# Kernel tuning notes

Hardware: AMD Instinct MI355X
Metric: run time of the kernel (lower is better)

Reference implementation:

```python
import jax, jax.numpy as jnp
import numpy as np

N_NODES = 100000
N_EDGES = 1600000
D_IN = 256
D_OUT = 256


def _init_linear(key, out_f, in_f):
    # torch nn.Linear default: U(-1/sqrt(in_f), 1/sqrt(in_f))
    kw, kb = jax.random.split(key)
    bound = 1.0 / np.sqrt(in_f)
    W = jax.random.uniform(kw, (out_f, in_f), jnp.float32, -bound, bound)
    b = jax.random.uniform(kb, (out_f,), jnp.float32, -bound, bound)
    return W, b


def setup_inputs() -> dict:
    key = jax.random.key(0)
    ks = jax.random.split(key, 7)
    x = jax.random.normal(ks[0], (N_NODES, D_IN), jnp.float32)
    edge_index = jax.random.randint(ks[1], (2, N_EDGES), 0, N_NODES, jnp.int64)
    W1, b1 = _init_linear(ks[2], D_OUT, D_IN)
    W2, b2 = _init_linear(ks[3], D_OUT // 2, D_OUT)
    W3, b3 = _init_linear(ks[4], D_OUT // 2, D_OUT)
    Wd1, bd1 = _init_linear(ks[5], D_OUT, D_OUT)
    Wd2, bd2 = _init_linear(ks[6], 1, D_OUT)
    return {"x": x, "edge_index": edge_index,
            "W1": W1, "b1": b1, "W2": W2, "b2": b2, "W3": W3, "b3": b3,
            "Wd1": Wd1, "bd1": bd1, "Wd2": Wd2, "bd2": bd2}


def _l2norm(x):
    return x / jnp.linalg.norm(x, axis=-1, keepdims=True)


def reference(x, edge_index, W1, b1, W2, b2, W3, b3, Wd1, bd1, Wd2, bd2):
    src, dst = edge_index[0], edge_index[1]  # source_to_target flow
    x = jax.nn.relu(x @ W1.T + b1)           # [N, D_OUT]
    x = _l2norm(x)
    for _ in range(2):
        # sum-aggregate neighbor messages: scatter-add x[src] into dst
        nm = jax.ops.segment_sum(x[src], dst, num_segments=N_NODES)  # [N, D_OUT]
        x = jax.nn.relu(jnp.concatenate([x @ W2.T + b2, nm @ W3.T + b3], axis=-1))
        x = _l2norm(x)
    x = jax.nn.relu(x @ Wd1.T + bd1)
    return x @ Wd2.T + bd2                    # [N, 1]
```

## Files before the change

kernel.cpp:

```cpp
#include <hip/hip_runtime.h>
#include <math.h>


typedef _Float16 f16x8 __attribute__((ext_vector_type(8)));
typedef float    f32x16 __attribute__((ext_vector_type(16)));

constexpr int DIM = 256;
constexpr int BM  = 128;
constexpr int BK  = 32;
constexpr int SA  = 40;
constexpr int SW  = 40;

__device__ __forceinline__ unsigned pk_hi2(float a, float b) {
    unsigned short ha = __builtin_bit_cast(unsigned short, (_Float16)a);
    unsigned short hb = __builtin_bit_cast(unsigned short, (_Float16)b);
    return (unsigned)ha | ((unsigned)hb << 16);
}
__device__ __forceinline__ unsigned pk_lo2(float a, float b) {
    _Float16 ha = (_Float16)a, hb = (_Float16)b;
    unsigned short la = __builtin_bit_cast(unsigned short, (_Float16)(a - (float)ha));
    unsigned short lb = __builtin_bit_cast(unsigned short, (_Float16)(b - (float)hb));
    return (unsigned)la | ((unsigned)lb << 16);
}
__device__ __forceinline__ unsigned pack_pair(float v) {
    _Float16 hi = (_Float16)v;
    _Float16 lo = (_Float16)(v - (float)hi);
    return (unsigned)__builtin_bit_cast(unsigned short, hi)
         | ((unsigned)__builtin_bit_cast(unsigned short, lo) << 16);
}

template <int AMODE, int EPI>
__device__ __forceinline__
void gemm_body(const void* __restrict__ Av,
               const float* __restrict__ WA, const float* __restrict__ WB,
               const float* __restrict__ bA, const float* __restrict__ bB,
               void* __restrict__ outv,
               const float* __restrict__ wd2, const float* __restrict__ bd2,
               float* __restrict__ out1, int M)
{
    __shared__ __align__(16) _Float16 smem[30720];
    _Float16* As_hi = smem;
    _Float16* As_lo = smem + 5120;
    _Float16* Ws_hi = smem + 10240;
    _Float16* Ws_lo = smem + 20480;

    const int tid  = threadIdx.x;
    const int lane = tid & 63;
    const int w    = tid >> 6;
    const int rh   = w >> 1;
    const int ch   = w & 1;
    const int l31  = lane & 31;
    const int lh   = lane >> 5;
    const int bm0  = blockIdx.x * BM;

    const unsigned* Au = (const unsigned*)Av;
    const int srow = tid >> 3;
    const int sch  = (tid & 7) * 4;

    uint4  pa[4];
    float4 pw[8];

    auto fetchA = [&](int t) {
        const int k0 = t * BK;
        #pragma unroll
        for (int i = 0; i < 4; ++i) {
            const int gr = bm0 + srow + 32 * i;
            uint4 v = {0u, 0u, 0u, 0u};
            if (gr < M) v = *(const uint4*)&Au[(size_t)gr * 256 + k0 + sch];
            pa[i] = v;
        }
    };
    auto fetchW = [&](int t) {
        const int k0 = t * BK;
        #pragma unroll
        for (int i = 0; i < 8; ++i) {
            const int r = srow + 32 * i;
            const float* src = (r < 128) ? &WA[(size_t)r * 256]
                                         : &WB[(size_t)(r - 128) * 256];
            pw[i] = *(const float4*)&src[k0 + sch];
        }
    };
    auto stageA = [&]() {
        #pragma unroll
        for (int i = 0; i < 4; ++i) {
            const int r = srow + 32 * i;
            unsigned h0, h1, l0, l1;
            if (AMODE == 0) {
                const float x0 = __builtin_bit_cast(float, pa[i].x);
                const float x1 = __builtin_bit_cast(float, pa[i].y);
                const float x2 = __builtin_bit_cast(float, pa[i].z);
                const float x3 = __builtin_bit_cast(float, pa[i].w);
                h0 = pk_hi2(x0, x1); h1 = pk_hi2(x2, x3);
                l0 = pk_lo2(x0, x1); l1 = pk_lo2(x2, x3);
            } else {
                h0 = __builtin_amdgcn_perm(pa[i].y, pa[i].x, 0x05040100u);
                l0 = __builtin_amdgcn_perm(pa[i].y, pa[i].x, 0x07060302u);
                h1 = __builtin_amdgcn_perm(pa[i].w, pa[i].z, 0x05040100u);
                l1 = __builtin_amdgcn_perm(pa[i].w, pa[i].z, 0x07060302u);
            }
            uint2 th; th.x = h0; th.y = h1;
            uint2 tl; tl.x = l0; tl.y = l1;
            *(uint2*)&As_hi[r * SA + sch] = th;
            *(uint2*)&As_lo[r * SA + sch] = tl;
        }
    };
    auto stageW = [&]() {
        #pragma unroll
        for (int i = 0; i < 8; ++i) {
            const int r = srow + 32 * i;
            uint2 th; th.x = pk_hi2(pw[i].x, pw[i].y); th.y = pk_hi2(pw[i].z, pw[i].w);
            uint2 tl; tl.x = pk_lo2(pw[i].x, pw[i].y); tl.y = pk_lo2(pw[i].z, pw[i].w);
            *(uint2*)&Ws_hi[r * SW + sch] = th;
            *(uint2*)&Ws_lo[r * SW + sch] = tl;
        }
    };

    f32x16 acc[2][4];
    #pragma unroll
    for (int tr = 0; tr < 2; ++tr)
        #pragma unroll
        for (int tc = 0; tc < 4; ++tc)
            #pragma unroll
            for (int i = 0; i < 16; ++i) acc[tr][tc][i] = 0.0f;

    fetchA(0); fetchW(0);

    #pragma unroll 1
    for (int t = 0; t < DIM / BK; ++t) {
        stageA(); stageW();
        __syncthreads();
        if (t < DIM / BK - 1) { fetchA(t + 1); fetchW(t + 1); }

        #pragma unroll
        for (int ks = 0; ks < 2; ++ks) {
            f16x8 ah[2], al[2], wh[4], wl[4];
            #pragma unroll
            for (int tr = 0; tr < 2; ++tr) {
                const int off = (rh * 64 + tr * 32 + l31) * SA + ks * 16 + lh * 8;
                ah[tr] = *(const f16x8*)&As_hi[off];
                al[tr] = *(const f16x8*)&As_lo[off];
            }
            #pragma unroll
            for (int tc = 0; tc < 4; ++tc) {
                const int off = (ch * 128 + tc * 32 + l31) * SW + ks * 16 + lh * 8;
                wh[tc] = *(const f16x8*)&Ws_hi[off];
                wl[tc] = *(const f16x8*)&Ws_lo[off];
            }
            #pragma unroll
            for (int tr = 0; tr < 2; ++tr)
                #pragma unroll
                for (int tc = 0; tc < 4; ++tc) {
                    acc[tr][tc] = __builtin_amdgcn_mfma_f32_32x32x16_f16(ah[tr], wh[tc], acc[tr][tc], 0, 0, 0);
                    acc[tr][tc] = __builtin_amdgcn_mfma_f32_32x32x16_f16(ah[tr], wl[tc], acc[tr][tc], 0, 0, 0);
                    acc[tr][tc] = __builtin_amdgcn_mfma_f32_32x32x16_f16(al[tr], wh[tc], acc[tr][tc], 0, 0, 0);
                }
        }
        __syncthreads();
    }


    if (EPI == 0) {
        float* z = (float*)outv;
        #pragma unroll
        for (int tr = 0; tr < 2; ++tr)
            #pragma unroll
            for (int i = 0; i < 16; ++i) {
                const int r  = rh * 64 + tr * 32 + 4 * lh + (i & 3) + 8 * (i >> 2);
                const int gr = bm0 + r;
                if (gr < M) {
                    #pragma unroll
                    for (int tc = 0; tc < 4; ++tc)
                        z[(size_t)gr * 256 + ch * 128 + tc * 32 + l31] = acc[tr][tc][i];
                }
            }
        return;
    }

    {
        float bias[4];
        #pragma unroll
        for (int tc = 0; tc < 4; ++tc)
            bias[tc] = (ch ? bB : bA)[tc * 32 + l31];
        #pragma unroll
        for (int tr = 0; tr < 2; ++tr)
            #pragma unroll
            for (int tc = 0; tc < 4; ++tc)
                #pragma unroll
                for (int i = 0; i < 16; ++i)
                    acc[tr][tc][i] = fmaxf(acc[tr][tc][i] + bias[tc], 0.0f);
    }

    float* red = (float*)smem;

    if (EPI == 1) {
        float ss[2][16];
        #pragma unroll
        for (int tr = 0; tr < 2; ++tr)
            #pragma unroll
            for (int i = 0; i < 16; ++i) {
                float s = 0.f;
                #pragma unroll
                for (int tc = 0; tc < 4; ++tc) s += acc[tr][tc][i] * acc[tr][tc][i];
                #pragma unroll
                for (int m = 1; m < 32; m <<= 1) s += __shfl_xor(s, m);
                ss[tr][i] = s;
            }
        const int j  = l31;
        const int ji = j & 15, jt = j >> 4;
        red[ch * 128 + rh * 64 + jt * 32 + 4 * lh + (ji & 3) + 8 * (ji >> 2)] = ss[jt][ji];
        __syncthreads();

        unsigned* hp = (unsigned*)outv;
        #pragma unroll
        for (int tr = 0; tr < 2; ++tr)
            #pragma unroll
            for (int i = 0; i < 16; ++i) {
                const int rl = rh * 64 + tr * 32 + 4 * lh + (i & 3) + 8 * (i >> 2);
                const float inv = 1.0f / sqrtf(red[rl] + red[128 + rl]);
                const int gr = bm0 + rl;
                if (gr < M) {
                    #pragma unroll
                    for (int tc = 0; tc < 4; ++tc)
                        hp[(size_t)gr * 256 + ch * 128 + tc * 32 + l31] =
                            pack_pair(acc[tr][tc][i] * inv);
                }
            }
        return;
    }

    {
        float wv[4];
        #pragma unroll
        for (int tc = 0; tc < 4; ++tc) wv[tc] = wd2[ch * 128 + tc * 32 + l31];
        float dd[2][16];
        #pragma unroll
        for (int tr = 0; tr < 2; ++tr)
            #pragma unroll
            for (int i = 0; i < 16; ++i) {
                float s = 0.f;
                #pragma unroll
                for (int tc = 0; tc < 4; ++tc) s += acc[tr][tc][i] * wv[tc];
                #pragma unroll
                for (int m = 1; m < 32; m <<= 1) s += __shfl_xor(s, m);
                dd[tr][i] = s;
            }
        const int j  = l31;
        const int ji = j & 15, jt = j >> 4;
        red[ch * 128 + rh * 64 + jt * 32 + 4 * lh + (ji & 3) + 8 * (ji >> 2)] = dd[jt][ji];
        __syncthreads();
        if (tid < 128) {
            const int gr = bm0 + tid;
            if (gr < M) out1[gr] = red[tid] + red[128 + tid] + bd2[0];
        }
    }
}

__global__ __launch_bounds__(256, 2)
void gemm_l1(const void* __restrict__ Av,
             const float* __restrict__ WA, const float* __restrict__ WB,
             const float* __restrict__ bA, const float* __restrict__ bB,
             void* __restrict__ outv, int M, int gb,
             const int* __restrict__ ei, int E, int* __restrict__ cnt)
{
    if ((int)blockIdx.x < gb) {
        gemm_body<0, 1>(Av, WA, WB, bA, bB, outv, nullptr, nullptr, nullptr, M);
    } else {
        const int base = ((int)blockIdx.x - gb) * 1024 + threadIdx.x;
        #pragma unroll
        for (int k = 0; k < 4; ++k) {
            const int e = base + k * 256;
            if (e < E) atomicAdd(&cnt[ei[E + e]], 1);
        }
    }
}

template <int DO_FILL>
__global__ __launch_bounds__(256, 2)
void gemm_z(const void* __restrict__ Av,
            const float* __restrict__ WA, const float* __restrict__ WB,
            void* __restrict__ outv, int M, int gb,
            const int* __restrict__ ei, int E,
            int* __restrict__ cursor, int* __restrict__ esrc)
{
    if ((int)blockIdx.x < gb) {
        gemm_body<1, 0>(Av, WA, WB, nullptr, nullptr, outv, nullptr, nullptr, nullptr, M);
    } else if (DO_FILL) {
        const int base = ((int)blockIdx.x - gb) * 1024 + threadIdx.x;
        #pragma unroll
        for (int k = 0; k < 4; ++k) {
            const int e = base + k * 256;
            if (e < E) {
                int d = ei[E + e];
                int p = atomicAdd(&cursor[d], 1);
                esrc[p] = ei[e];
            }
        }
    }
}

__global__ __launch_bounds__(256, 2)
void gemm_head(const void* __restrict__ Av,
               const float* __restrict__ WA, const float* __restrict__ WB,
               const float* __restrict__ bA, const float* __restrict__ bB,
               const float* __restrict__ wd2, const float* __restrict__ bd2,
               float* __restrict__ out1, int M)
{
    gemm_body<1, 2>(Av, WA, WB, bA, bB, nullptr, wd2, bd2, out1, M);
}


__global__ void scan1_kernel(const int* __restrict__ cnt, int n,
                             int* __restrict__ rp, int* __restrict__ sums)
{
    __shared__ int sm[1024];
    const int tid = threadIdx.x;
    const int i = blockIdx.x * 1024 + tid;
    const int v = (i < n) ? cnt[i] : 0;
    sm[tid] = v;
    __syncthreads();
    for (int off = 1; off < 1024; off <<= 1) {
        int t = (tid >= off) ? sm[tid - off] : 0;
        __syncthreads();
        sm[tid] += t;
        __syncthreads();
    }
    if (i < n) rp[i] = sm[tid] - v;
    if (tid == 1023) sums[blockIdx.x] = sm[tid];
}

__global__ void scan2_kernel(int* __restrict__ sums, int n)
{
    __shared__ int sm[128];
    const int tid = threadIdx.x;
    const int v = (tid < n) ? sums[tid] : 0;
    sm[tid] = v;
    __syncthreads();
    for (int off = 1; off < 128; off <<= 1) {
        int t = (tid >= off) ? sm[tid - off] : 0;
        __syncthreads();
        sm[tid] += t;
        __syncthreads();
    }
    if (tid < n) sums[tid] = sm[tid] - v;
}

__global__ void scan3_kernel(int* __restrict__ rp, const int* __restrict__ sums,
                             int* __restrict__ cursor, int n, int E)
{
    int i = blockIdx.x * blockDim.x + threadIdx.x;
    if (i < n) {
        int v = rp[i] + sums[i >> 10];
        rp[i] = v;
        cursor[i] = v;
    }
    if (i == 0) rp[n] = E;
}

__global__ __launch_bounds__(256)
void fin_kernel(const float* __restrict__ z, const int* __restrict__ rp,
                const int* __restrict__ esrc,
                const float* __restrict__ b2, const float* __restrict__ b3,
                unsigned* __restrict__ hp, int M)
{
    const int v    = blockIdx.x * 4 + (threadIdx.x >> 6);
    const int lane = threadIdx.x & 63;
    if (v >= M) return;
    const int beg = rp[v], end = rp[v + 1];
    const int deg = end - beg;

    const float2 z1 = *(const float2*)&z[(size_t)v * DIM + lane * 2];
    const float2 c2 = *(const float2*)&b2[lane * 2];
    const float2 c3 = *(const float2*)&b3[lane * 2];

    const float* z2 = z + 128;
    float ax0 = 0.f, ay0 = 0.f, ax1 = 0.f, ay1 = 0.f;
    float ax2 = 0.f, ay2 = 0.f, ax3 = 0.f, ay3 = 0.f;

    for (int base = 0; base < deg; base += 64) {
        const int cnt = min(64, deg - base);
        int myidx = 0;
        if (lane < cnt) myidx = esrc[beg + base + lane];
        int j = 0;
        for (; j + 3 < cnt; j += 4) {
            const int s0 = __builtin_amdgcn_readlane(myidx, j);
            const int s1 = __builtin_amdgcn_readlane(myidx, j + 1);
            const int s2 = __builtin_amdgcn_readlane(myidx, j + 2);
            const int s3 = __builtin_amdgcn_readlane(myidx, j + 3);
            const float2 g0 = *(const float2*)&z2[(size_t)s0 * DIM + lane * 2];
            const float2 g1 = *(const float2*)&z2[(size_t)s1 * DIM + lane * 2];
            const float2 g2 = *(const float2*)&z2[(size_t)s2 * DIM + lane * 2];
            const float2 g3 = *(const float2*)&z2[(size_t)s3 * DIM + lane * 2];
            ax0 += g0.x; ay0 += g0.y;
            ax1 += g1.x; ay1 += g1.y;
            ax2 += g2.x; ay2 += g2.y;
            ax3 += g3.x; ay3 += g3.y;
        }
        for (; j < cnt; ++j) {
            const int s0 = __builtin_amdgcn_readlane(myidx, j);
            const float2 g0 = *(const float2*)&z2[(size_t)s0 * DIM + lane * 2];
            ax0 += g0.x; ay0 += g0.y;
        }
    }
    const float sx = (ax0 + ax1) + (ax2 + ax3);
    const float sy = (ay0 + ay1) + (ay2 + ay3);

    const float u1x = fmaxf(z1.x + c2.x, 0.f), u1y = fmaxf(z1.y + c2.y, 0.f);
    const float u2x = fmaxf(sx + c3.x, 0.f),  u2y = fmaxf(sy + c3.y, 0.f);

    float ss = u1x * u1x + u1y * u1y + u2x * u2x + u2y * u2y;
    #pragma unroll
    for (int off = 32; off > 0; off >>= 1) ss += __shfl_xor(ss, off);
    const float inv = 1.0f / sqrtf(ss);

    uint2 p1; p1.x = pack_pair(u1x * inv); p1.y = pack_pair(u1y * inv);
    uint2 p2; p2.x = pack_pair(u2x * inv); p2.y = pack_pair(u2y * inv);
    *(uint2*)&hp[(size_t)v * DIM + lane * 2]       = p1;
    *(uint2*)&hp[(size_t)v * DIM + 128 + lane * 2] = p2;
}


extern "C" void kernel_launch(void* const* d_in, const int* in_sizes, int n_in,
                              void* d_out, int out_size, void* d_ws, size_t ws_size,
                              hipStream_t stream)
{
    const float* x   = (const float*)d_in[0];
    const int*   ei  = (const int*)d_in[1];
    const float* W1  = (const float*)d_in[2];
    const float* b1  = (const float*)d_in[3];
    const float* W2  = (const float*)d_in[4];
    const float* b2  = (const float*)d_in[5];
    const float* W3  = (const float*)d_in[6];
    const float* b3  = (const float*)d_in[7];
    const float* Wd1 = (const float*)d_in[8];
    const float* bd1 = (const float*)d_in[9];
    const float* Wd2 = (const float*)d_in[10];
    const float* bd2 = (const float*)d_in[11];
    float* out = (float*)d_out;

    const int M = in_sizes[0] / DIM;
    const int E = in_sizes[1] / 2;

    unsigned* hp  = (unsigned*)d_ws;
    float*    z   = (float*)(hp + (size_t)M * DIM);
    int*   rp     = (int*)(z + (size_t)M * DIM);
    int*   cursor = rp + (M + 1);
    int*   esrc   = cursor + M;
    int*   sums   = esrc + E;

    hipMemsetAsync(cursor, 0, sizeof(int) * M, stream);

    const int gb  = (M + BM - 1) / BM;
    const int hb  = (E + 1023) / 1024;
    const int nb1 = (M + 1023) / 1024;
    const int fb  = (M + 3) / 4;

    gemm_l1<<<gb + hb, 256, 0, stream>>>(
        x, W1, W1 + 128 * DIM, b1, b1 + 128, hp, M, gb, ei, E, cursor);

    scan1_kernel<<<nb1, 1024, 0, stream>>>(cursor, M, rp, sums);
    scan2_kernel<<<1, 128, 0, stream>>>(sums, nb1);
    scan3_kernel<<<(M + 255) / 256, 256, 0, stream>>>(rp, sums, cursor, M, E);

    gemm_z<1><<<gb + hb, 256, 0, stream>>>(hp, W2, W3, z, M, gb, ei, E, cursor, esrc);
    fin_kernel<<<fb, 256, 0, stream>>>(z, rp, esrc, b2, b3, hp, M);

    gemm_z<0><<<gb, 256, 0, stream>>>(hp, W2, W3, z, M, gb, nullptr, 0, nullptr, nullptr);
    fin_kernel<<<fb, 256, 0, stream>>>(z, rp, esrc, b2, b3, hp, M);

    gemm_head<<<gb, 256, 0, stream>>>(
        hp, Wd1, Wd1 + 128 * DIM, bd1, bd1 + 128, Wd2, bd2, out, M);
}
```

Measured before the change: 733.9 us.

## Use 512-thread GEMM blocks with 2x4 wave grid and direct-load W staging

Each GEMM block now runs 8 waves arranged 2x4, so every wave holds a 64x64 accumulator tile instead of 64x128. This halves accumulator registers per thread so more waves fit per CU. W tiles are no longer prefetched into registers; they are loaded and converted inside the loop just before the sync. The row-norm and head reductions switch to a four-way per-row partial layout, and the edge-histogram blocks are resized to match. The trade-off is that W global loads are no longer overlapped with MFMA work, and more waves compete for LDS bandwidth on the same tile.

```diff
diff --git a/kernel.cpp b/kernel.cpp
--- a/kernel.cpp
+++ b/kernel.cpp
@@ -9,7 +9,6 @@
 constexpr int BM  = 128;
 constexpr int BK  = 32;
 constexpr int SA  = 40;
-constexpr int SW  = 40;
 
 __device__ __forceinline__ unsigned pk_hi2(float a, float b) {
     unsigned short ha = __builtin_bit_cast(unsigned short, (_Float16)a);
@@ -44,112 +43,111 @@
     _Float16* Ws_hi = smem + 10240;
     _Float16* Ws_lo = smem + 20480;
 
-    const int tid  = threadIdx.x;
-    const int lane = tid & 63;
-    const int w    = tid >> 6;
-    const int rh   = w >> 1;
-    const int ch   = w & 1;
-    const int l31  = lane & 31;
-    const int lh   = lane >> 5;
-    const int bm0  = blockIdx.x * BM;
+    const int tid = threadIdx.x;
+    const int l31 = tid & 31;
+    const int lh  = (tid >> 5) & 1;
+    const int w   = tid >> 6;
+    const int wr  = w >> 2;
+    const int wc  = w & 3;
+    const int bm0 = blockIdx.x * BM;
 
     const unsigned* Au = (const unsigned*)Av;
-    const int srow = tid >> 3;
-    const int sch  = (tid & 7) * 4;
-
-    uint4  pa[4];
-    float4 pw[8];
-
+    const int srow = tid >> 2;
+    const int sch  = (tid & 3) * 8;
+    const int srw  = tid >> 1;
+    const int scw  = (tid & 1) * 16;
+
+    uint4 pa[2];
     auto fetchA = [&](int t) {
         const int k0 = t * BK;
-        #pragma unroll
-        for (int i = 0; i < 4; ++i) {
-            const int gr = bm0 + srow + 32 * i;
-            uint4 v = {0u, 0u, 0u, 0u};
-            if (gr < M) v = *(const uint4*)&Au[(size_t)gr * 256 + k0 + sch];
-            pa[i] = v;
-        }
-    };
-    auto fetchW = [&](int t) {
-        const int k0 = t * BK;
-        #pragma unroll
-        for (int i = 0; i < 8; ++i) {
-            const int r = srow + 32 * i;
-            const float* src = (r < 128) ? &WA[(size_t)r * 256]
-                                         : &WB[(size_t)(r - 128) * 256];
-            pw[i] = *(const float4*)&src[k0 + sch];
+        const int gr = bm0 + srow;
+        if (gr < M) {
+            pa[0] = *(const uint4*)&Au[(size_t)gr * 256 + k0 + sch];
+            pa[1] = *(const uint4*)&Au[(size_t)gr * 256 + k0 + sch + 4];
+        } else {
+            pa[0] = uint4{0u,0u,0u,0u}; pa[1] = uint4{0u,0u,0u,0u};
         }
     };
     auto stageA = [&]() {
-        #pragma unroll
-        for (int i = 0; i < 4; ++i) {
-            const int r = srow + 32 * i;
-            unsigned h0, h1, l0, l1;
-            if (AMODE == 0) {
-                const float x0 = __builtin_bit_cast(float, pa[i].x);
-                const float x1 = __builtin_bit_cast(float, pa[i].y);
-                const float x2 = __builtin_bit_cast(float, pa[i].z);
-                const float x3 = __builtin_bit_cast(float, pa[i].w);
-                h0 = pk_hi2(x0, x1); h1 = pk_hi2(x2, x3);
-                l0 = pk_lo2(x0, x1); l1 = pk_lo2(x2, x3);
-            } else {
-                h0 = __builtin_amdgcn_perm(pa[i].y, pa[i].x, 0x05040100u);
-                l0 = __builtin_amdgcn_perm(pa[i].y, pa[i].x, 0x07060302u);
-                h1 = __builtin_amdgcn_perm(pa[i].w, pa[i].z, 0x05040100u);
-                l1 = __builtin_amdgcn_perm(pa[i].w, pa[i].z, 0x07060302u);
-            }
-            uint2 th; th.x = h0; th.y = h1;
-            uint2 tl; tl.x = l0; tl.y = l1;
-            *(uint2*)&As_hi[r * SA + sch] = th;
-            *(uint2*)&As_lo[r * SA + sch] = tl;
-        }
+        uint4 hi, lo;
+        if (AMODE == 0) {
+            const float x0 = __builtin_bit_cast(float, pa[0].x);
+            const float x1 = __builtin_bit_cast(float, pa[0].y);
+            const float x2 = __builtin_bit_cast(float, pa[0].z);
+            const float x3 = __builtin_bit_cast(float, pa[0].w);
+            const float x4 = __builtin_bit_cast(float, pa[1].x);
+            const float x5 = __builtin_bit_cast(float, pa[1].y);
+            const float x6 = __builtin_bit_cast(float, pa[1].z);
+            const float x7 = __builtin_bit_cast(float, pa[1].w);
+            hi = uint4{pk_hi2(x0,x1), pk_hi2(x2,x3), pk_hi2(x4,x5), pk_hi2(x6,x7)};
+            lo = uint4{pk_lo2(x0,x1), pk_lo2(x2,x3), pk_lo2(x4,x5), pk_lo2(x6,x7)};
+        } else {
+            hi = uint4{__builtin_amdgcn_perm(pa[0].y, pa[0].x, 0x05040100u),
+                       __builtin_amdgcn_perm(pa[0].w, pa[0].z, 0x05040100u),
+                       __builtin_amdgcn_perm(pa[1].y, pa[1].x, 0x05040100u),
+                       __builtin_amdgcn_perm(pa[1].w, pa[1].z, 0x05040100u)};
+            lo = uint4{__builtin_amdgcn_perm(pa[0].y, pa[0].x, 0x07060302u),
+                       __builtin_amdgcn_perm(pa[0].w, pa[0].z, 0x07060302u),
+                       __builtin_amdgcn_perm(pa[1].y, pa[1].x, 0x07060302u),
+                       __builtin_amdgcn_perm(pa[1].w, pa[1].z, 0x07060302u)};
+        }
+        *(uint4*)&As_hi[srow * SA + sch] = hi;
+        *(uint4*)&As_lo[srow * SA + sch] = lo;
     };
-    auto stageW = [&]() {
-        #pragma unroll
-        for (int i = 0; i < 8; ++i) {
-            const int r = srow + 32 * i;
-            uint2 th; th.x = pk_hi2(pw[i].x, pw[i].y); th.y = pk_hi2(pw[i].z, pw[i].w);
-            uint2 tl; tl.x = pk_lo2(pw[i].x, pw[i].y); tl.y = pk_lo2(pw[i].z, pw[i].w);
-            *(uint2*)&Ws_hi[r * SW + sch] = th;
-            *(uint2*)&Ws_lo[r * SW + sch] = tl;
-        }
+    auto stageW = [&](int t) {
+        const int k0 = t * BK;
+        const float* src = (srw < 128) ? &WA[(size_t)srw * 256]
+                                       : &WB[(size_t)(srw - 128) * 256];
+        const float4 w0 = *(const float4*)&src[k0 + scw];
+        const float4 w1 = *(const float4*)&src[k0 + scw + 4];
+        const float4 w2 = *(const float4*)&src[k0 + scw + 8];
+        const float4 w3 = *(const float4*)&src[k0 + scw + 12];
+        uint4 hi0{pk_hi2(w0.x,w0.y), pk_hi2(w0.z,w0.w), pk_hi2(w1.x,w1.y), pk_hi2(w1.z,w1.w)};
+        uint4 hi1{pk_hi2(w2.x,w2.y), pk_hi2(w2.z,w2.w), pk_hi2(w3.x,w3.y), pk_hi2(w3.z,w3.w)};
+        uint4 lo0{pk_lo2(w0.x,w0.y), pk_lo2(w0.z,w0.w), pk_lo2(w1.x,w1.y), pk_lo2(w1.z,w1.w)};
+        uint4 lo1{pk_lo2(w2.x,w2.y), pk_lo2(w2.z,w2.w), pk_lo2(w3.x,w3.y), pk_lo2(w3.z,w3.w)};
+        *(uint4*)&Ws_hi[srw * SA + scw]     = hi0;
+        *(uint4*)&Ws_hi[srw * SA + scw + 8] = hi1;
+        *(uint4*)&Ws_lo[srw * SA + scw]     = lo0;
+        *(uint4*)&Ws_lo[srw * SA + scw + 8] = lo1;
     };
 
-    f32x16 acc[2][4];
+    f32x16 acc[2][2];
     #pragma unroll
     for (int tr = 0; tr < 2; ++tr)
         #pragma unroll
-        for (int tc = 0; tc < 4; ++tc)
+        for (int tc = 0; tc < 2; ++tc)
             #pragma unroll
             for (int i = 0; i < 16; ++i) acc[tr][tc][i] = 0.0f;
 
-    fetchA(0); fetchW(0);
+    fetchA(0);
 
     #pragma unroll 1
     for (int t = 0; t < DIM / BK; ++t) {
-        stageA(); stageW();
-        __syncthreads();
-        if (t < DIM / BK - 1) { fetchA(t + 1); fetchW(t + 1); }
+        stageA();
+        stageW(t);
+        __syncthreads();
+        if (t < DIM / BK - 1) fetchA(t + 1);
 
         #pragma unroll
         for (int ks = 0; ks < 2; ++ks) {
-            f16x8 ah[2], al[2], wh[4], wl[4];
+            f16x8 ah[2], al[2], wh[2], wl[2];
             #pragma unroll
             for (int tr = 0; tr < 2; ++tr) {
-                const int off = (rh * 64 + tr * 32 + l31) * SA + ks * 16 + lh * 8;
+                const int off = (wr * 64 + tr * 32 + l31) * SA + ks * 16 + lh * 8;
                 ah[tr] = *(const f16x8*)&As_hi[off];
                 al[tr] = *(const f16x8*)&As_lo[off];
             }
             #pragma unroll
-            for (int tc = 0; tc < 4; ++tc) {
-                const int off = (ch * 128 + tc * 32 + l31) * SW + ks * 16 + lh * 8;
+            for (int tc = 0; tc < 2; ++tc) {
+                const int off = (wc * 64 + tc * 32 + l31) * SA + ks * 16 + lh * 8;
                 wh[tc] = *(const f16x8*)&Ws_hi[off];
                 wl[tc] = *(const f16x8*)&Ws_lo[off];
             }
             #pragma unroll
             for (int tr = 0; tr < 2; ++tr)
                 #pragma unroll
-                for (int tc = 0; tc < 4; ++tc) {
+                for (int tc = 0; tc < 2; ++tc) {
                     acc[tr][tc] = __builtin_amdgcn_mfma_f32_32x32x16_f16(ah[tr], wh[tc], acc[tr][tc], 0, 0, 0);
                     acc[tr][tc] = __builtin_amdgcn_mfma_f32_32x32x16_f16(ah[tr], wl[tc], acc[tr][tc], 0, 0, 0);
                     acc[tr][tc] = __builtin_amdgcn_mfma_f32_32x32x16_f16(al[tr], wh[tc], acc[tr][tc], 0, 0, 0);
@@ -165,26 +163,28 @@
         for (int tr = 0; tr < 2; ++tr)
             #pragma unroll
             for (int i = 0; i < 16; ++i) {
-                const int r  = rh * 64 + tr * 32 + 4 * lh + (i & 3) + 8 * (i >> 2);
+                const int r  = wr * 64 + tr * 32 + 4 * lh + (i & 3) + 8 * (i >> 2);
                 const int gr = bm0 + r;
                 if (gr < M) {
                     #pragma unroll
-                    for (int tc = 0; tc < 4; ++tc)
-                        z[(size_t)gr * 256 + ch * 128 + tc * 32 + l31] = acc[tr][tc][i];
+                    for (int tc = 0; tc < 2; ++tc)
+                        z[(size_t)gr * 256 + wc * 64 + tc * 32 + l31] = acc[tr][tc][i];
                 }
             }
         return;
     }
 
     {
-        float bias[4];
-        #pragma unroll
-        for (int tc = 0; tc < 4; ++tc)
-            bias[tc] = (ch ? bB : bA)[tc * 32 + l31];
+        float bias[2];
+        #pragma unroll
+        for (int tc = 0; tc < 2; ++tc) {
+            const int col = wc * 64 + tc * 32 + l31;
+            bias[tc] = (col < 128) ? bA[col] : bB[col - 128];
+        }
         #pragma unroll
         for (int tr = 0; tr < 2; ++tr)
             #pragma unroll
-            for (int tc = 0; tc < 4; ++tc)
+            for (int tc = 0; tc < 2; ++tc)
                 #pragma unroll
                 for (int i = 0; i < 16; ++i)
                     acc[tr][tc][i] = fmaxf(acc[tr][tc][i] + bias[tc], 0.0f);
@@ -193,21 +193,18 @@
     float* red = (float*)smem;
 
     if (EPI == 1) {
-        float ss[2][16];
         #pragma unroll
         for (int tr = 0; tr < 2; ++tr)
             #pragma unroll
             for (int i = 0; i < 16; ++i) {
-                float s = 0.f;
-                #pragma unroll
-                for (int tc = 0; tc < 4; ++tc) s += acc[tr][tc][i] * acc[tr][tc][i];
+                float s = acc[tr][0][i] * acc[tr][0][i] + acc[tr][1][i] * acc[tr][1][i];
                 #pragma unroll
                 for (int m = 1; m < 32; m <<= 1) s += __shfl_xor(s, m);
-                ss[tr][i] = s;
-            }
-        const int j  = l31;
-        const int ji = j & 15, jt = j >> 4;
-        red[ch * 128 + rh * 64 + jt * 32 + 4 * lh + (ji & 3) + 8 * (ji >> 2)] = ss[jt][ji];
+                if (l31 == tr * 16 + i) {
+                    const int r = wr * 64 + tr * 32 + 4 * lh + (i & 3) + 8 * (i >> 2);
+                    red[r * 4 + wc] = s;
+                }
+            }
         __syncthreads();
 
         unsigned* hp = (unsigned*)outv;
@@ -215,13 +212,14 @@
         for (int tr = 0; tr < 2; ++tr)
             #pragma unroll
             for (int i = 0; i < 16; ++i) {
-                const int rl = rh * 64 + tr * 32 + 4 * lh + (i & 3) + 8 * (i >> 2);
-                const float inv = 1.0f / sqrtf(red[rl] + red[128 + rl]);
+                const int rl = wr * 64 + tr * 32 + 4 * lh + (i & 3) + 8 * (i >> 2);
+                const float inv = 1.0f / sqrtf(red[rl * 4] + red[rl * 4 + 1] +
+                                               red[rl * 4 + 2] + red[rl * 4 + 3]);
                 const int gr = bm0 + rl;
                 if (gr < M) {
                     #pragma unroll
-                    for (int tc = 0; tc < 4; ++tc)
-                        hp[(size_t)gr * 256 + ch * 128 + tc * 32 + l31] =
+                    for (int tc = 0; tc < 2; ++tc)
+                        hp[(size_t)gr * 256 + wc * 64 + tc * 32 + l31] =
                             pack_pair(acc[tr][tc][i] * inv);
                 }
             }
@@ -229,33 +227,32 @@
     }
 
     {
-        float wv[4];
-        #pragma unroll
-        for (int tc = 0; tc < 4; ++tc) wv[tc] = wd2[ch * 128 + tc * 32 + l31];
-        float dd[2][16];
+        float wv[2];
+        #pragma unroll
+        for (int tc = 0; tc < 2; ++tc) wv[tc] = wd2[wc * 64 + tc * 32 + l31];
         #pragma unroll
         for (int tr = 0; tr < 2; ++tr)
             #pragma unroll
             for (int i = 0; i < 16; ++i) {
-                float s = 0.f;
-                #pragma unroll
-                for (int tc = 0; tc < 4; ++tc) s += acc[tr][tc][i] * wv[tc];
+                float s = acc[tr][0][i] * wv[0] + acc[tr][1][i] * wv[1];
                 #pragma unroll
                 for (int m = 1; m < 32; m <<= 1) s += __shfl_xor(s, m);
-                dd[tr][i] = s;
-            }
-        const int j  = l31;
-        const int ji = j & 15, jt = j >> 4;
-        red[ch * 128 + rh * 64 + jt * 32 + 4 * lh + (ji & 3) + 8 * (ji >> 2)] = dd[jt][ji];
+                if (l31 == tr * 16 + i) {
+                    const int r = wr * 64 + tr * 32 + 4 * lh + (i & 3) + 8 * (i >> 2);
+                    red[r * 4 + wc] = s;
+                }
+            }
         __syncthreads();
         if (tid < 128) {
             const int gr = bm0 + tid;
-            if (gr < M) out1[gr] = red[tid] + red[128 + tid] + bd2[0];
-        }
-    }
-}
-
-__global__ __launch_bounds__(256, 2)
+            if (gr < M)
+                out1[gr] = red[tid * 4] + red[tid * 4 + 1] + red[tid * 4 + 2] +
+                           red[tid * 4 + 3] + bd2[0];
+        }
+    }
+}
+
+__global__ __launch_bounds__(512, 4)
 void gemm_l1(const void* __restrict__ Av,
              const float* __restrict__ WA, const float* __restrict__ WB,
              const float* __restrict__ bA, const float* __restrict__ bB,
@@ -265,17 +262,17 @@
     if ((int)blockIdx.x < gb) {
         gemm_body<0, 1>(Av, WA, WB, bA, bB, outv, nullptr, nullptr, nullptr, M);
     } else {
-        const int base = ((int)blockIdx.x - gb) * 1024 + threadIdx.x;
+        const int base = ((int)blockIdx.x - gb) * 2048 + threadIdx.x;
         #pragma unroll
         for (int k = 0; k < 4; ++k) {
-            const int e = base + k * 256;
+            const int e = base + k * 512;
             if (e < E) atomicAdd(&cnt[ei[E + e]], 1);
         }
     }
 }
 
 template <int DO_FILL>
-__global__ __launch_bounds__(256, 2)
+__global__ __launch_bounds__(512, 4)
 void gemm_z(const void* __restrict__ Av,
             const float* __restrict__ WA, const float* __restrict__ WB,
             void* __restrict__ outv, int M, int gb,
@@ -285,10 +282,10 @@
     if ((int)blockIdx.x < gb) {
         gemm_body<1, 0>(Av, WA, WB, nullptr, nullptr, outv, nullptr, nullptr, nullptr, M);
     } else if (DO_FILL) {
-        const int base = ((int)blockIdx.x - gb) * 1024 + threadIdx.x;
+        const int base = ((int)blockIdx.x - gb) * 2048 + threadIdx.x;
         #pragma unroll
         for (int k = 0; k < 4; ++k) {
-            const int e = base + k * 256;
+            const int e = base + k * 512;
             if (e < E) {
                 int d = ei[E + e];
                 int p = atomicAdd(&cursor[d], 1);
@@ -298,7 +295,7 @@
     }
 }
 
-__global__ __launch_bounds__(256, 2)
+__global__ __launch_bounds__(512, 4)
 void gemm_head(const void* __restrict__ Av,
                const float* __restrict__ WA, const float* __restrict__ WB,
                const float* __restrict__ bA, const float* __restrict__ bB,
@@ -450,23 +447,23 @@
     hipMemsetAsync(cursor, 0, sizeof(int) * M, stream);
 
     const int gb  = (M + BM - 1) / BM;
-    const int hb  = (E + 1023) / 1024;
+    const int hb  = (E + 2047) / 2048;
     const int nb1 = (M + 1023) / 1024;
     const int fb  = (M + 3) / 4;
 
-    gemm_l1<<<gb + hb, 256, 0, stream>>>(
+    gemm_l1<<<gb + hb, 512, 0, stream>>>(
         x, W1, W1 + 128 * DIM, b1, b1 + 128, hp, M, gb, ei, E, cursor);
 
     scan1_kernel<<<nb1, 1024, 0, stream>>>(cursor, M, rp, sums);
     scan2_kernel<<<1, 128, 0, stream>>>(sums, nb1);
     scan3_kernel<<<(M + 255) / 256, 256, 0, stream>>>(rp, sums, cursor, M, E);
 
-    gemm_z<1><<<gb + hb, 256, 0, stream>>>(hp, W2, W3, z, M, gb, ei, E, cursor, esrc);
+    gemm_z<1><<<gb + hb, 512, 0, stream>>>(hp, W2, W3, z, M, gb, ei, E, cursor, esrc);
     fin_kernel<<<fb, 256, 0, stream>>>(z, rp, esrc, b2, b3, hp, M);
 
-    gemm_z<0><<<gb, 256, 0, stream>>>(hp, W2, W3, z, M, gb, nullptr, 0, nullptr, nullptr);
+    gemm_z<0><<<gb, 512, 0, stream>>>(hp, W2, W3, z, M, gb, nullptr, 0, nullptr, nullptr);
     fin_kernel<<<fb, 256, 0, stream>>>(z, rp, esrc, b2, b3, hp, M);
 
-    gemm_head<<<gb, 256, 0, stream>>>(
+    gemm_head<<<gb, 512, 0, stream>>>(
         hp, Wd1, Wd1 + 128 * DIM, bd1, bd1 + 128, Wd2, bd2, out, M);
 }
```

Result: no change. 748.1 us (+1.9%).
